# Optimization experiments

Hardware: AMD Instinct MI355X
Metric: run time of the kernel (lower is better)

Reference implementation:

```python
import jax, jax.numpy as jnp
import numpy as np

B, S, HID = 1, 2048, 4096
NH, NKV, HD = 32, 8, 128
EPS = 1e-6
SCALE = HD ** -0.5


def _rope_cos_sin(seq_len, head_dim, base=1000000.0):
    inv_freq = 1.0 / (base ** (np.arange(0, head_dim, 2, dtype=np.float32) / head_dim))
    t = np.arange(seq_len, dtype=np.float32)
    freqs = np.outer(t, inv_freq)                      # [S, HD/2]
    emb = np.concatenate([freqs, freqs], axis=-1)       # [S, HD]
    return jnp.asarray(np.cos(emb))[None], jnp.asarray(np.sin(emb))[None]  # [1,S,HD]


def setup_inputs() -> dict:
    key = jax.random.key(0)
    ks = jax.random.split(key, 8)
    cos, sin = _rope_cos_sin(S, HD)
    inp = {
        "hidden_states": jax.random.normal(ks[0], (B, S, HID), jnp.float32),
        "cos": jnp.broadcast_to(cos, (B, S, HD)),
        "sin": jnp.broadcast_to(sin, (B, S, HD)),
        "Wq": jax.random.normal(ks[1], (NH * HD, HID), jnp.float32) * 0.02,
        "Wk": jax.random.normal(ks[2], (NKV * HD, HID), jnp.float32) * 0.02,
        "Wv": jax.random.normal(ks[3], (NKV * HD, HID), jnp.float32) * 0.02,
        "Wo": jax.random.normal(ks[4], (HID, NH * HD), jnp.float32) * 0.02,
        "q_norm_w": jnp.ones((HD,), jnp.float32),
        "k_norm_w": jnp.ones((HD,), jnp.float32),
    }
    return inp


def _rmsnorm(x, w, eps=EPS):
    var = jnp.mean(jnp.square(x), axis=-1, keepdims=True)
    return x * jax.lax.rsqrt(var + eps) * w


def _rotate_half(x):
    x1, x2 = jnp.split(x, 2, axis=-1)
    return jnp.concatenate([-x2, x1], axis=-1)


def _apply_rope(x, cos, sin):
    # x: [b,s,n,d]; cos/sin: [b,s,d] -> unsqueeze head dim (dim=2)
    c = cos[:, :, None, :]
    s = sin[:, :, None, :]
    return x * c + _rotate_half(x) * s


def reference(hidden_states, cos, sin, Wq, Wk, Wv, Wo, q_norm_w, k_norm_w):
    b, s, _ = hidden_states.shape
    q = (hidden_states @ Wq.T).reshape(b, s, NH, HD)
    k = (hidden_states @ Wk.T).reshape(b, s, NKV, HD)
    v = (hidden_states @ Wv.T).reshape(b, s, NKV, HD)
    # per-head RMSNorm on q and k
    q = _rmsnorm(q, q_norm_w)
    k = _rmsnorm(k, k_norm_w)
    # RoPE
    q = _apply_rope(q, cos, sin)
    k = _apply_rope(k, cos, sin)
    # GQA: expand kv heads to match query heads (group size = NH // NKV)
    g = NH // NKV
    k = jnp.repeat(k, g, axis=2)  # [b,s,NH,d]
    v = jnp.repeat(v, g, axis=2)
    # causal SDPA, layout bsnd
    scores = jnp.einsum("bqhd,bkhd->bhqk", q, k) * SCALE
    causal = jnp.tril(jnp.ones((s, s), dtype=bool))
    scores = jnp.where(causal[None, None], scores, jnp.finfo(scores.dtype).min)
    probs = jax.nn.softmax(scores, axis=-1)
    attn = jnp.einsum("bhqk,bkhd->bqhd", probs, v).reshape(b, s, NH * HD)
    return attn @ Wo.T
```

## Files before the change

### kernel.cpp

```cpp
#include <hip/hip_runtime.h>
#include <hip/hip_bf16.h>
#include <stdint.h>

#define S_LEN 2048
#define HIDD  4096
#define NH    32
#define NKV   8
#define HD    128
#define NQKV  6144
#define ATT_SCALE 0.08838834764831845f
#define LOG2E 1.4426950408889634f

typedef unsigned short u16;
typedef __attribute__((ext_vector_type(8))) short short8;
typedef __attribute__((ext_vector_type(4))) float f32x4;

__device__ __forceinline__ unsigned f2bfbits(float f){
  union{float f; unsigned u;} v; v.f = f;
  return (v.u + 0x7FFFu + ((v.u>>16)&1u)) >> 16;
}
__device__ __forceinline__ float bf2f(u16 b){
  union{unsigned u; float f;} v; v.u = ((unsigned)b)<<16;
  return v.f;
}
__device__ __forceinline__ unsigned packbf(float a, float b){
  return f2bfbits(a) | (f2bfbits(b)<<16);
}
__device__ __forceinline__ unsigned cvtpk(float lo, float hi){
  unsigned r;
  asm("v_cvt_pk_bf16_f32 %0, %1, %2" : "=v"(r) : "v"(lo), "v"(hi));
  return r;
}

#define GLOAD16(g, l) __builtin_amdgcn_global_load_lds( \
    (__attribute__((address_space(1))) void*)(g), \
    (__attribute__((address_space(3))) void*)(l), 16, 0, 0)

#define VMWAIT(n) asm volatile("s_waitcnt vmcnt(" #n ")" ::: "memory")
#define SCHED0() __builtin_amdgcn_sched_barrier(0)

__global__ __launch_bounds__(256) void cvt_all(const float* __restrict__ hs,
                                               const float* __restrict__ Wq,
                                               const float* __restrict__ Wk,
                                               const float* __restrict__ Wv,
                                               u16* __restrict__ Xb,
                                               u16* __restrict__ WQKV){
  const float* src; u16* dst; int n8;
  switch (blockIdx.y){
    case 0: src = hs; dst = Xb;                        n8 = S_LEN*HIDD/8;    break;
    case 1: src = Wq; dst = WQKV;                      n8 = NH*HD*HIDD/8;    break;
    case 2: src = Wk; dst = WQKV + (size_t)NH*HD*HIDD; n8 = NKV*HD*HIDD/8;   break;
    default:src = Wv; dst = WQKV + (size_t)(NH+NKV)*HD*HIDD; n8 = NKV*HD*HIDD/8; break;
  }
  int i = blockIdx.x*256 + threadIdx.x;
  if (i >= n8) return;
  const float4* p = (const float4*)src;
  float4 a = p[2*i], b = p[2*i+1];
  union { unsigned u[4]; short8 s; } o;
  o.u[0] = packbf(a.x, a.y); o.u[1] = packbf(a.z, a.w);
  o.u[2] = packbf(b.x, b.y); o.u[3] = packbf(b.z, b.w);
  *(short8*)(dst + (size_t)i*8) = o.s;
}

__global__ __launch_bounds__(256) void cvt_bf16(const float* __restrict__ in,
                                                u16* __restrict__ out, int n8){
  int i = blockIdx.x*256 + threadIdx.x;
  if (i >= n8) return;
  const float4* p = (const float4*)in;
  float4 a = p[2*i], b = p[2*i+1];
  union { unsigned u[4]; short8 s; } o;
  o.u[0] = packbf(a.x, a.y); o.u[1] = packbf(a.z, a.w);
  o.u[2] = packbf(b.x, b.y); o.u[3] = packbf(b.z, b.w);
  *(short8*)(out + (size_t)i*8) = o.s;
}

template<int BM, int BN, typename OT>
__global__ __launch_bounds__(512) void gemm_4ph(const u16* __restrict__ A,
                                                const u16* __restrict__ B,
                                                OT* __restrict__ C,
                                                int N, int K, int nbx){
  constexpr int MREP = BM/32;
  constexpr int NF   = BN/64;
  constexpr int AH   = BM/128;
  constexpr int ASZ  = BM*64;
  __shared__ __align__(16) char lds[4*ASZ + 65536];

  const int tid = threadIdx.x;
  const int w = tid>>6, lane = tid&63, ln = lane&15, g = lane>>4;
  const int wm = w>>2, wn = w&3;
  const int swz5 = ((ln>>3)&1)<<5;

  const int nwg = gridDim.x, flat = blockIdx.x;
  const int wg = (flat&7)*(nwg>>3) + (flat>>3);
  const int by = wg/nbx, bx = wg - by*nbx;
  const int m0 = by*BM, n0 = bx*BN;

  const int rs   = ((tid>>6)<<4) + ((tid&63)>>2);
  const int ksrc = ((tid&3)<<3) ^ (((tid>>5)&1)<<4);
  const u16* srcA[AH];
  #pragma unroll
  for (int h=0;h<AH;h++) srcA[h] = A + (size_t)(m0 + h*128 + rs)*K + ksrc;
  const u16* srcB[2];
  #pragma unroll
  for (int h=0;h<2;h++)  srcB[h] = B + (size_t)(n0 + h*128 + rs)*K + ksrc;

  #define AREG(bf,kh) (lds + ((bf)*2 + (kh))*ASZ)
  #define BREG(bf,kh) (lds + 4*ASZ + ((bf)*2 + (kh))*16384)

  #define STAGEPT(t, kh, bf) { const int off_ = (t)*64 + (kh)*32;                 \
    _Pragma("unroll") for (int h=0;h<AH;h++)                                      \
      GLOAD16(srcA[h]+off_, AREG(bf,kh) + h*8192 + w*1024);                       \
    _Pragma("unroll") for (int h=0;h<2;h++)                                       \
      GLOAD16(srcB[h]+off_, BREG(bf,kh) + h*8192 + w*1024); }

  f32x4 acc[MREP][NF];
  #pragma unroll
  for (int m=0;m<MREP;m++)
    #pragma unroll
    for (int n=0;n<NF;n++) acc[m][n] = (f32x4){0.f,0.f,0.f,0.f};
  short8 a_[MREP], b_[NF];

  #define READA(bf,kh) { _Pragma("unroll") for (int m=0;m<MREP;m++)               \
    a_[m] = *(const short8*)(AREG(bf,kh) + (wm*MREP+m)*1024 + ln*64 + ((g*16)^swz5)); }
  #define READB(bf,kh) { _Pragma("unroll") for (int n=0;n<NF;n++)                 \
    b_[n] = *(const short8*)(BREG(bf,kh) + (wn*NF+n)*1024 + ln*64 + ((g*16)^swz5)); }
  #define MFMACLU() { __builtin_amdgcn_s_setprio(1);                              \
    _Pragma("unroll") for (int m=0;m<MREP;m++)                                    \
      _Pragma("unroll") for (int n=0;n<NF;n++)                                    \
        acc[m][n] = __builtin_amdgcn_mfma_f32_16x16x32_bf16(a_[m], b_[n], acc[m][n], 0,0,0); \
    __builtin_amdgcn_s_setprio(0); }
  #define BARR() __builtin_amdgcn_s_barrier()
  #define VM2LP() do{ if constexpr (AH==2) { VMWAIT(8); } else { VMWAIT(6); } }while(0)
  #define VM1LP() do{ if constexpr (AH==2) { VMWAIT(4); } else { VMWAIT(3); } }while(0)

  STAGEPT(0,0,0); STAGEPT(0,1,0); STAGEPT(1,0,1);
  VMWAIT(0); BARR(); SCHED0();

  const int NIT = K>>7;
  #pragma unroll 1
  for (int it=0; it<NIT; ++it){
    const bool last = (it == NIT-1);
    const int t0 = 2*it;
    READB(0,0); READA(0,0); STAGEPT(t0+1, 1, 1);
    MFMACLU();
    SCHED0(); VM2LP(); BARR(); SCHED0();
    READB(0,1); READA(0,1); if (!last) STAGEPT(t0+2, 0, 0);
    MFMACLU();
    SCHED0(); if (last) { VM1LP(); } else { VM2LP(); } BARR(); SCHED0();
    READB(1,0); READA(1,0); if (!last) STAGEPT(t0+2, 1, 0);
    MFMACLU();
    SCHED0(); if (last) { VMWAIT(0); } else { VM2LP(); } BARR(); SCHED0();
    READB(1,1); READA(1,1); if (!last) STAGEPT(t0+3, 0, 1);
    MFMACLU();
    SCHED0(); if (!last) { VM2LP(); } BARR(); SCHED0();
  }

  #pragma unroll
  for (int mi=0; mi<MREP; mi++)
    #pragma unroll
    for (int n=0; n<NF; n++)
      #pragma unroll
      for (int r=0;r<4;r++){
        int row = m0 + (wm*MREP+mi)*16 + g*4 + r;
        int col = n0 + wn*(NF*16) + n*16 + ln;
        if constexpr (__is_same(OT, u16))
          C[(size_t)row*N + col] = (u16)f2bfbits(acc[mi][n][r]);
        else
          C[(size_t)row*N + col] = acc[mi][n][r];
      }
  #undef AREG
  #undef BREG
  #undef STAGEPT
  #undef READA
  #undef READB
  #undef MFMACLU
  #undef BARR
  #undef VM2LP
  #undef VM1LP
}

__global__ __launch_bounds__(256) void norm_rope(const u16* __restrict__ QKVb,
                                                 const float* __restrict__ cosb,
                                                 const float* __restrict__ sinb,
                                                 const float* __restrict__ qw,
                                                 const float* __restrict__ kw,
                                                 u16* __restrict__ Qn,
                                                 u16* __restrict__ Kn,
                                                 u16* __restrict__ Vt){
  int w = threadIdx.x>>6, lane = threadIdx.x&63;
  int row = blockIdx.x*4 + w;
  int s = row / 48, slot = row - s*48;
  const u16* src = QKVb + (size_t)s*NQKV + slot*HD;
  float x0 = bf2f(src[lane]), x1 = bf2f(src[lane+64]);
  if (slot < 40){
    float ss = x0*x0 + x1*x1;
    #pragma unroll
    for (int off=1; off<64; off<<=1) ss += __shfl_xor(ss, off, 64);
    float r = rsqrtf(ss*(1.0f/128.0f) + 1e-6f);
    const float* wgt = (slot < 32) ? qw : kw;
    float y0 = x0*r*wgt[lane], y1 = x1*r*wgt[lane+64];
    float c0 = cosb[(size_t)s*HD+lane], c1 = cosb[(size_t)s*HD+lane+64];
    float s0 = sinb[(size_t)s*HD+lane], s1 = sinb[(size_t)s*HD+lane+64];
    float o0 = y0*c0 - y1*s0;
    float o1 = y1*c1 + y0*s1;
    float sc = (slot < 32) ? (ATT_SCALE*LOG2E) : 1.0f;
    u16* dst = (slot < 32) ? (Qn + ((size_t)slot*S_LEN + s)*HD)
                           : (Kn + ((size_t)(slot-32)*S_LEN + s)*HD);
    dst[lane]    = (u16)f2bfbits(o0*sc);
    dst[lane+64] = (u16)f2bfbits(o1*sc);
  } else {
    int kvh = slot - 40;
    u16* dst = Vt + (size_t)kvh*HD*S_LEN + s;
    dst[(size_t)lane*S_LEN]      = (u16)f2bfbits(x0);
    dst[(size_t)(lane+64)*S_LEN] = (u16)f2bfbits(x1);
  }
}

__global__ __launch_bounds__(256) void flash_attn(const u16* __restrict__ Qn,
                                                  const u16* __restrict__ Kn,
                                                  const u16* __restrict__ Vt,
                                                  u16* __restrict__ O){
  __shared__ u16 Ks[2][64*128];
  __shared__ u16 Vs[2][128*64];

  const int h = blockIdx.y;
  const int w = threadIdx.x>>6, lane = threadIdx.x&63, ln = lane&15, g = lane>>4;
  const int kvh = h>>2;
  const u16* Qh = Qn + (size_t)h*S_LEN*HD;
  const u16* Kh = Kn + (size_t)kvh*S_LEN*HD;
  const u16* Vh = Vt + (size_t)kvh*HD*S_LEN;

  const int krow_w = w*4 + g;
  const int ksw    = ((krow_w)&7)<<4;
  const int kcol   = ((ln*16) ^ ksw) >> 1;
  const int vrow_w = w*8 + (lane>>3);
  const int vsw    = ((lane>>3)&7)<<4;
  const int vcol   = (((lane&7)*16) ^ vsw) >> 1;

  #define STAGE_K(bufi, t) { \
    int kv0_ = (t)*64; \
    _Pragma("unroll") \
    for (int p=0;p<4;p++){ \
      const u16* ga = Kh + (size_t)(kv0_ + p*16 + krow_w)*HD + kcol; \
      GLOAD16(ga, (char*)&Ks[bufi][0] + p*4096 + w*1024); \
    } \
  }
  #define STAGE_V(bufi, t) { \
    int kv0_ = (t)*64; \
    _Pragma("unroll") \
    for (int p=0;p<4;p++){ \
      const u16* gv = Vh + (size_t)(p*32 + vrow_w)*S_LEN + kv0_ + vcol; \
      GLOAD16(gv, (char*)&Vs[bufi][0] + p*4096 + w*1024); \
    } \
  }

  #pragma unroll 1
  for (int ph=0; ph<2; ph++){
    const int qb = ph ? (31 - blockIdx.x) : blockIdx.x;
    const int q0 = qb*64;
    const int qrow = q0 + w*16 + ln;

    short8 qf[4];
    #pragma unroll
    for (int c=0;c<4;c++)
      qf[c] = *(const short8*)(Qh + (size_t)qrow*HD + c*32 + g*8);

    f32x4 ot[8];
    #pragma unroll
    for (int dt=0;dt<8;dt++) ot[dt] = (f32x4){0.f,0.f,0.f,0.f};
    float m_run = -1e30f, l_run = 0.f;

    const int nt = qb + 1;

    STAGE_K(0, 0); STAGE_V(0, 0);
    __syncthreads();

    for (int t=0; t<nt; ++t){
      const int cur = t&1;
      if (t+1 < nt) STAGE_K(cur^1, t+1);
      const int kv0 = t*64;

      f32x4 st[4];
      #pragma unroll
      for (int mt=0; mt<4; mt++){
        short8 kf[4];
        #pragma unroll
        for (int c=0;c<4;c++)
          kf[c] = *(const short8*)((const char*)&Ks[cur][0]
                      + (mt*16+ln)*256 + ((c*64 + g*16) ^ ((ln&7)<<4)));
        f32x4 acc = (f32x4){0.f,0.f,0.f,0.f};
        __builtin_amdgcn_s_setprio(1);
        #pragma unroll
        for (int c=0;c<4;c++)
          acc = __builtin_amdgcn_mfma_f32_16x16x32_bf16(kf[c], qf[c], acc, 0,0,0);
        __builtin_amdgcn_s_setprio(0);
        st[mt] = acc;
      }

      if (t+1 < nt) STAGE_V(cur^1, t+1);

      float p[4][4];
      float mtile = -1e30f;
      if (t < qb){
        #pragma unroll
        for (int mt=0; mt<4; mt++)
          #pragma unroll
          for (int r=0;r<4;r++){
            p[mt][r] = st[mt][r];
            mtile = fmaxf(mtile, st[mt][r]);
          }
      } else {
        #pragma unroll
        for (int mt=0; mt<4; mt++)
          #pragma unroll
          for (int r=0;r<4;r++){
            int kv = kv0 + mt*16 + 4*g + r;
            float sv = (kv <= qrow) ? st[mt][r] : -1e30f;
            p[mt][r] = sv;
            mtile = fmaxf(mtile, sv);
          }
      }
      mtile = fmaxf(mtile, __shfl_xor(mtile, 16, 64));
      mtile = fmaxf(mtile, __shfl_xor(mtile, 32, 64));

      bool defer = __all(mtile <= m_run + 11.5416f);
      float m_new = defer ? m_run : fmaxf(m_run, mtile);

      float l_tile = 0.f;
      #pragma unroll
      for (int mt=0; mt<4; mt++)
        #pragma unroll
        for (int r=0;r<4;r++){
          float e = exp2f(p[mt][r] - m_new);
          p[mt][r] = e;
          l_tile += e;
        }
      l_tile += __shfl_xor(l_tile, 16, 64);
      l_tile += __shfl_xor(l_tile, 32, 64);
      if (defer){
        l_run += l_tile;
      } else {
        float alpha = exp2f(m_run - m_new);
        l_run = l_run*alpha + l_tile;
        m_run = m_new;
        #pragma unroll
        for (int dt=0;dt<8;dt++) ot[dt] *= alpha;
      }

      short8 pf[2];
      #pragma unroll
      for (int ks2=0; ks2<2; ks2++){
        unsigned pk00 = cvtpk(p[2*ks2  ][0], p[2*ks2  ][1]);
        unsigned pk01 = cvtpk(p[2*ks2  ][2], p[2*ks2  ][3]);
        unsigned pk10 = cvtpk(p[2*ks2+1][0], p[2*ks2+1][1]);
        unsigned pk11 = cvtpk(p[2*ks2+1][2], p[2*ks2+1][3]);
        int src0 = (((2*g  )&3)<<4) | ln;
        int src1 = (((2*g+1)&3)<<4) | ln;
        unsigned t00 = (unsigned)__shfl((int)pk00, src0, 64);
        unsigned t10 = (unsigned)__shfl((int)pk10, src0, 64);
        unsigned t01 = (unsigned)__shfl((int)pk01, src0, 64);
        unsigned t11 = (unsigned)__shfl((int)pk11, src0, 64);
        unsigned u00 = (unsigned)__shfl((int)pk00, src1, 64);
        unsigned u10 = (unsigned)__shfl((int)pk10, src1, 64);
        unsigned u01 = (unsigned)__shfl((int)pk01, src1, 64);
        unsigned u11 = (unsigned)__shfl((int)pk11, src1, 64);
        bool hiv = (g >= 2);
        union { unsigned u[4]; short8 s; } pw;
        pw.u[0] = hiv ? t10 : t00;
        pw.u[1] = hiv ? t11 : t01;
        pw.u[2] = hiv ? u10 : u00;
        pw.u[3] = hiv ? u11 : u01;
        pf[ks2] = pw.s;
      }

      #pragma unroll
      for (int dt=0;dt<8;dt++){
        short8 vf[2];
        #pragma unroll
        for (int ks2=0; ks2<2; ks2++)
          vf[ks2] = *(const short8*)((const char*)&Vs[cur][0]
                      + (dt*16+ln)*128 + ((ks2*64 + g*16) ^ ((ln&7)<<4)));
        __builtin_amdgcn_s_setprio(1);
        #pragma unroll
        for (int ks2=0; ks2<2; ks2++)
          ot[dt] = __builtin_amdgcn_mfma_f32_16x16x32_bf16(vf[ks2], pf[ks2], ot[dt], 0,0,0);
        __builtin_amdgcn_s_setprio(0);
      }
      __syncthreads();
    }

    float inv = 1.0f / l_run;
    u16* orow = O + (size_t)qrow*(NH*HD) + h*HD;
    #pragma unroll
    for (int dt=0;dt<8;dt++){
      #pragma unroll
      for (int rr=0; rr<4; rr+=2){
        unsigned pkd = cvtpk(ot[dt][rr]*inv, ot[dt][rr+1]*inv);
        *(unsigned*)(orow + dt*16 + g*4 + rr) = pkd;
      }
    }
  }
  #undef STAGE_K
  #undef STAGE_V
}

extern "C" void kernel_launch(void* const* d_in, const int* in_sizes, int n_in,
                              void* d_out, int out_size, void* d_ws, size_t ws_size,
                              hipStream_t stream){
  (void)in_sizes; (void)n_in; (void)out_size; (void)ws_size;
  const float* hs   = (const float*)d_in[0];
  const float* cosb = (const float*)d_in[1];
  const float* sinb = (const float*)d_in[2];
  const float* Wq   = (const float*)d_in[3];
  const float* Wk   = (const float*)d_in[4];
  const float* Wv   = (const float*)d_in[5];
  const float* Wo   = (const float*)d_in[6];
  const float* qw   = (const float*)d_in[7];
  const float* kw   = (const float*)d_in[8];
  float* out = (float*)d_out;

  char* ws = (char*)d_ws;
  u16*   Xb    = (u16*)  (ws);
  u16*   WQKV  = (u16*)  (ws + 16777216);
  u16*   QKVb  = (u16*)  (ws + 67108864);
  u16*   attnB = (u16*)  (ws + 94371840);
  u16*   Qn    = (u16*)  (ws + 117440512);
  u16*   Kn    = (u16*)  (ws + 134217728);
  u16*   Vt    = (u16*)  (ws + 138412032);
  u16*   Wob   = WQKV;

  cvt_all<<<dim3(8192, 4), 256, 0, stream>>>(hs, Wq, Wk, Wv, Xb, WQKV);
  gemm_4ph<256,192,u16><<<256, 512, 0, stream>>>(Xb, WQKV, QKVb, NQKV, HIDD, NQKV/192);
  norm_rope<<<(S_LEN*48)/4, 256, 0, stream>>>(QKVb, cosb, sinb, qw, kw, Qn, Kn, Vt);
  cvt_bf16<<<(HIDD*NH*HD/8)/256, 256, 0, stream>>>(Wo, Wob, HIDD*NH*HD/8);
  flash_attn<<<dim3(16, NH), 256, 0, stream>>>(Qn, Kn, Vt, attnB);
  gemm_4ph<128,256,float><<<256, 512, 0, stream>>>(attnB, Wob, out, HIDD, HIDD, HIDD/256);
}
```

Baseline: 330.0 us.

## Split-K output projection with larger tiles and a separate reduction kernel

The output projection GEMM moves from 128x256 tiles over the full K to 256x256 tiles with a split-K factor of 2. This keeps the workgroup count at 256 while raising operand reuse per tile. Each half writes a bf16 partial into spare workspace, and a new elementwise kernel sums the two partials into the fp32 output. The trade-off is an extra kernel launch and extra memory traffic for the partials. Storing intermediate sums in bf16 also adds rounding error.

```diff
diff --git a/kernel.cpp b/kernel.cpp
--- a/kernel.cpp
+++ b/kernel.cpp
@@ -74,11 +74,32 @@
   *(short8*)(out + (size_t)i*8) = o.s;
 }
 
-template<int BM, int BN, typename OT>
+__global__ __launch_bounds__(256) void reduce_add(const u16* __restrict__ P0,
+                                                  const u16* __restrict__ P1,
+                                                  float* __restrict__ out, int n8){
+  int i = blockIdx.x*256 + threadIdx.x;
+  if (i >= n8) return;
+  short8 a = *(const short8*)(P0 + (size_t)i*8);
+  short8 b = *(const short8*)(P1 + (size_t)i*8);
+  float4 o0, o1;
+  o0.x = bf2f((u16)a[0]) + bf2f((u16)b[0]);
+  o0.y = bf2f((u16)a[1]) + bf2f((u16)b[1]);
+  o0.z = bf2f((u16)a[2]) + bf2f((u16)b[2]);
+  o0.w = bf2f((u16)a[3]) + bf2f((u16)b[3]);
+  o1.x = bf2f((u16)a[4]) + bf2f((u16)b[4]);
+  o1.y = bf2f((u16)a[5]) + bf2f((u16)b[5]);
+  o1.z = bf2f((u16)a[6]) + bf2f((u16)b[6]);
+  o1.w = bf2f((u16)a[7]) + bf2f((u16)b[7]);
+  float4* po = (float4*)(out + (size_t)i*8);
+  po[0] = o0; po[1] = o1;
+}
+
+template<int BM, int BN, int KS, typename OT>
 __global__ __launch_bounds__(512) void gemm_4ph(const u16* __restrict__ A,
                                                 const u16* __restrict__ B,
-                                                OT* __restrict__ C,
-                                                int N, int K, int nbx){
+                                                OT* __restrict__ C0,
+                                                OT* __restrict__ C1,
+                                                int N, int Kstride, int nbx){
   constexpr int MREP = BM/32;
   constexpr int NF   = BN/64;
   constexpr int AH   = BM/128;
@@ -92,17 +113,22 @@
 
   const int nwg = gridDim.x, flat = blockIdx.x;
   const int wg = (flat&7)*(nwg>>3) + (flat>>3);
-  const int by = wg/nbx, bx = wg - by*nbx;
+  const int ntile = nwg / KS;
+  const int ks = wg / ntile;
+  const int tb = wg - ks*ntile;
+  const int by = tb/nbx, bx = tb - by*nbx;
   const int m0 = by*BM, n0 = bx*BN;
+  const int Kext = Kstride / KS;
+  const size_t koff = (size_t)ks * Kext;
 
   const int rs   = ((tid>>6)<<4) + ((tid&63)>>2);
   const int ksrc = ((tid&3)<<3) ^ (((tid>>5)&1)<<4);
   const u16* srcA[AH];
   #pragma unroll
-  for (int h=0;h<AH;h++) srcA[h] = A + (size_t)(m0 + h*128 + rs)*K + ksrc;
+  for (int h=0;h<AH;h++) srcA[h] = A + (size_t)(m0 + h*128 + rs)*Kstride + koff + ksrc;
   const u16* srcB[2];
   #pragma unroll
-  for (int h=0;h<2;h++)  srcB[h] = B + (size_t)(n0 + h*128 + rs)*K + ksrc;
+  for (int h=0;h<2;h++)  srcB[h] = B + (size_t)(n0 + h*128 + rs)*Kstride + koff + ksrc;
 
   #define AREG(bf,kh) (lds + ((bf)*2 + (kh))*ASZ)
   #define BREG(bf,kh) (lds + 4*ASZ + ((bf)*2 + (kh))*16384)
@@ -136,7 +162,7 @@
   STAGEPT(0,0,0); STAGEPT(0,1,0); STAGEPT(1,0,1);
   VMWAIT(0); BARR(); SCHED0();
 
-  const int NIT = K>>7;
+  const int NIT = Kext>>7;
   #pragma unroll 1
   for (int it=0; it<NIT; ++it){
     const bool last = (it == NIT-1);
@@ -155,6 +181,7 @@
     SCHED0(); if (!last) { VM2LP(); } BARR(); SCHED0();
   }
 
+  OT* Cw = (KS == 2 && ks == 1) ? C1 : C0;
   #pragma unroll
   for (int mi=0; mi<MREP; mi++)
     #pragma unroll
@@ -164,9 +191,9 @@
         int row = m0 + (wm*MREP+mi)*16 + g*4 + r;
         int col = n0 + wn*(NF*16) + n*16 + ln;
         if constexpr (__is_same(OT, u16))
-          C[(size_t)row*N + col] = (u16)f2bfbits(acc[mi][n][r]);
+          Cw[(size_t)row*N + col] = (u16)f2bfbits(acc[mi][n][r]);
         else
-          C[(size_t)row*N + col] = acc[mi][n][r];
+          Cw[(size_t)row*N + col] = acc[mi][n][r];
       }
   #undef AREG
   #undef BREG
@@ -428,11 +455,14 @@
   u16*   Kn    = (u16*)  (ws + 134217728);
   u16*   Vt    = (u16*)  (ws + 138412032);
   u16*   Wob   = WQKV;
+  u16*   P0    = Xb;
+  u16*   P1    = QKVb;
 
   cvt_all<<<dim3(8192, 4), 256, 0, stream>>>(hs, Wq, Wk, Wv, Xb, WQKV);
-  gemm_4ph<256,192,u16><<<256, 512, 0, stream>>>(Xb, WQKV, QKVb, NQKV, HIDD, NQKV/192);
+  gemm_4ph<256,192,1,u16><<<256, 512, 0, stream>>>(Xb, WQKV, QKVb, nullptr, NQKV, HIDD, NQKV/192);
   norm_rope<<<(S_LEN*48)/4, 256, 0, stream>>>(QKVb, cosb, sinb, qw, kw, Qn, Kn, Vt);
   cvt_bf16<<<(HIDD*NH*HD/8)/256, 256, 0, stream>>>(Wo, Wob, HIDD*NH*HD/8);
   flash_attn<<<dim3(16, NH), 256, 0, stream>>>(Qn, Kn, Vt, attnB);
-  gemm_4ph<128,256,float><<<256, 512, 0, stream>>>(attnB, Wob, out, HIDD, HIDD, HIDD/256);
-}
+  gemm_4ph<256,256,2,u16><<<256, 512, 0, stream>>>(attnB, Wob, P0, P1, HIDD, HIDD, HIDD/256);
+  reduce_add<<<(S_LEN*HIDD/8)/256, 256, 0, stream>>>(P0, P1, out, S_LEN*HIDD/8);
+}
```

Result: no change. 331.3 us (+0.4%).

## Double-buffer MFMA operand registers to overlap LDS reads with matrix math

Applied to the files above, without the earlier changes.

The GEMM main loop now keeps two sets of A/B fragment registers. It reads the next k-half's fragments from LDS before issuing MFMAs on the current set, instead of reading and then immediately computing. The vmcnt waits are retuned and the barrier schedule is reworked around this earlier read, including a prologue read before the loop. This is meant to hide LDS read latency behind MFMA execution. In exchange it uses more VGPRs, which could lower occupancy, and it makes the LDS buffer hazards across barriers harder to get right.

```diff
diff --git a/kernel.cpp b/kernel.cpp
--- a/kernel.cpp
+++ b/kernel.cpp
@@ -118,41 +118,45 @@
   for (int m=0;m<MREP;m++)
     #pragma unroll
     for (int n=0;n<NF;n++) acc[m][n] = (f32x4){0.f,0.f,0.f,0.f};
-  short8 a_[MREP], b_[NF];
-
-  #define READA(bf,kh) { _Pragma("unroll") for (int m=0;m<MREP;m++)               \
-    a_[m] = *(const short8*)(AREG(bf,kh) + (wm*MREP+m)*1024 + ln*64 + ((g*16)^swz5)); }
-  #define READB(bf,kh) { _Pragma("unroll") for (int n=0;n<NF;n++)                 \
-    b_[n] = *(const short8*)(BREG(bf,kh) + (wn*NF+n)*1024 + ln*64 + ((g*16)^swz5)); }
-  #define MFMACLU() { __builtin_amdgcn_s_setprio(1);                              \
+  short8 a0_[MREP], b0_[NF], a1_[MREP], b1_[NF];
+
+  #define READ_SET(aset, bset, bf, kh) {                                          \
+    _Pragma("unroll") for (int n=0;n<NF;n++)                                      \
+      bset[n] = *(const short8*)(BREG(bf,kh) + (wn*NF+n)*1024 + ln*64 + ((g*16)^swz5)); \
+    _Pragma("unroll") for (int m=0;m<MREP;m++)                                    \
+      aset[m] = *(const short8*)(AREG(bf,kh) + (wm*MREP+m)*1024 + ln*64 + ((g*16)^swz5)); }
+  #define MFMA_SET(aset, bset) { __builtin_amdgcn_s_setprio(1);                   \
     _Pragma("unroll") for (int m=0;m<MREP;m++)                                    \
       _Pragma("unroll") for (int n=0;n<NF;n++)                                    \
-        acc[m][n] = __builtin_amdgcn_mfma_f32_16x16x32_bf16(a_[m], b_[n], acc[m][n], 0,0,0); \
+        acc[m][n] = __builtin_amdgcn_mfma_f32_16x16x32_bf16(aset[m], bset[n], acc[m][n], 0,0,0); \
     __builtin_amdgcn_s_setprio(0); }
   #define BARR() __builtin_amdgcn_s_barrier()
-  #define VM2LP() do{ if constexpr (AH==2) { VMWAIT(8); } else { VMWAIT(6); } }while(0)
-  #define VM1LP() do{ if constexpr (AH==2) { VMWAIT(4); } else { VMWAIT(3); } }while(0)
+  #define VMST() do{ if constexpr (AH==2) { VMWAIT(4); } else { VMWAIT(3); } }while(0)
 
   STAGEPT(0,0,0); STAGEPT(0,1,0); STAGEPT(1,0,1);
   VMWAIT(0); BARR(); SCHED0();
+  READ_SET(a0_, b0_, 0, 0);
 
   const int NIT = K>>7;
   #pragma unroll 1
   for (int it=0; it<NIT; ++it){
     const bool last = (it == NIT-1);
     const int t0 = 2*it;
-    READB(0,0); READA(0,0); STAGEPT(t0+1, 1, 1);
-    MFMACLU();
-    SCHED0(); VM2LP(); BARR(); SCHED0();
-    READB(0,1); READA(0,1); if (!last) STAGEPT(t0+2, 0, 0);
-    MFMACLU();
-    SCHED0(); if (last) { VM1LP(); } else { VM2LP(); } BARR(); SCHED0();
-    READB(1,0); READA(1,0); if (!last) STAGEPT(t0+2, 1, 0);
-    MFMACLU();
-    SCHED0(); if (last) { VMWAIT(0); } else { VM2LP(); } BARR(); SCHED0();
-    READB(1,1); READA(1,1); if (!last) STAGEPT(t0+3, 0, 1);
-    MFMACLU();
-    SCHED0(); if (!last) { VM2LP(); } BARR(); SCHED0();
+    READ_SET(a1_, b1_, 0, 1);
+    STAGEPT(t0+1, 1, 1);
+    MFMA_SET(a0_, b0_);
+    SCHED0(); VMST(); BARR(); SCHED0();
+    READ_SET(a0_, b0_, 1, 0);
+    if (!last) STAGEPT(t0+2, 0, 0);
+    MFMA_SET(a1_, b1_);
+    SCHED0(); if (last) { VMWAIT(0); } else { VMST(); } BARR(); SCHED0();
+    READ_SET(a1_, b1_, 1, 1);
+    if (!last) STAGEPT(t0+2, 1, 0);
+    MFMA_SET(a0_, b0_);
+    SCHED0(); if (!last) { VMST(); } BARR(); SCHED0();
+    if (!last){ READ_SET(a0_, b0_, 0, 0); STAGEPT(t0+3, 0, 1); }
+    MFMA_SET(a1_, b1_);
+    if (!last){ SCHED0(); VMST(); BARR(); SCHED0(); }
   }
 
   #pragma unroll
@@ -171,12 +175,10 @@
   #undef AREG
   #undef BREG
   #undef STAGEPT
-  #undef READA
-  #undef READB
-  #undef MFMACLU
+  #undef READ_SET
+  #undef MFMA_SET
   #undef BARR
-  #undef VM2LP
-  #undef VM1LP
+  #undef VMST
 }
 
 __global__ __launch_bounds__(256) void norm_rope(const u16* __restrict__ QKVb,
```

Result: no change. 329.6 us (-0.1%).
